# Performance work log

Measured on AMD Instinct MI355X. Metric: run time of the kernel, lower is better.

## Reference

```python
import jax, jax.numpy as jnp
import numpy as np

B, C, H, W = 32, 128, 12, 12
L = H * W
D = C + 1            # +1 coordinate channel
HID = 64

def leaky(x):
    return jax.nn.leaky_relu(x, negative_slope=0.01)

def setup_inputs() -> dict:
    key = jax.random.key(0)
    ks = jax.random.split(key, 9)
    def lin(k, fin, fout):
        bound = 1.0 / np.sqrt(fin)
        kw, kb = jax.random.split(k)
        Wt = jax.random.uniform(kw, (fin, fout), minval=-bound, maxval=bound, dtype=jnp.float32)
        bb = jax.random.uniform(kb, (fout,), minval=-bound, maxval=bound, dtype=jnp.float32)
        return Wt, bb
    x_img = jax.random.normal(ks[0], (B, C, H, W), dtype=jnp.float32)
    W1, b1 = lin(ks[1], 2 * D, HID)
    W2, b2 = lin(ks[2], HID, HID)
    Wp, bp = lin(ks[3], HID, HID)
    Wo, bo = lin(ks[4], HID, HID)
    return {"x_img": x_img, "W1": W1, "b1": b1, "W2": W2, "b2": b2,
            "Wp": Wp, "bp": bp, "Wo": Wo, "bo": bo}

def reference(x_img, W1, b1, W2, b2, Wp, bp, Wo, bo):
    b, c, h, w = x_img.shape
    length = h * w
    # [b, L, c]
    x = x_img.reshape(b, c, length).transpose(0, 2, 1)
    coords = jnp.broadcast_to(jnp.arange(length, dtype=x.dtype)[None, :, None], (b, length, 1))
    x = jnp.concatenate([x, coords], axis=2)            # [b, L, D]
    # pair feature is concat([x_i, x_j]) where x_i[b,i,j]=x[b,j], x_j[b,i,j]=x[b,i].
    # Linear on concat == split-weight sum; avoids materializing [b,L,L,2D].
    Wa, Wb = W1[:D], W1[D:]
    gi = jnp.einsum('bld,dh->blh', x, Wa)               # contribution of x_i (indexed by j)
    gj = jnp.einsum('bld,dh->blh', x, Wb)               # contribution of x_j (indexed by i)
    g = leaky(gi[:, None, :, :] + gj[:, :, None, :] + b1)   # [b, L, L, HID]
    g = leaky(jnp.einsum('bijh,hk->bijk', g, W2) + b2)       # [b, L, L, HID]
    out = g.sum(axis=(1, 2))                                 # [b, HID]
    out = leaky(out @ Wp + bp)
    out = leaky(out @ Wo + bo)
    return out
```

## Files before the change

kernel.cpp:

```cpp
#include <hip/hip_runtime.h>


#define B_   32
#define C_   128
#define L_   144
#define HID_ 64
#define D_   129
#define STR  68
#define YB_  18

typedef __bf16 bf16x8 __attribute__((ext_vector_type(8)));
typedef float  floatx4 __attribute__((ext_vector_type(4)));

__device__ __forceinline__ float leaky(float x) { return fmaxf(x, 0.01f * x); }
__device__ __forceinline__ floatx4 leaky4(floatx4 x) {
    return __builtin_elementwise_max(x, x * 0.01f);
}

__global__ __launch_bounds__(256) void k_proj(const float* __restrict__ x_img,
                                              const float* __restrict__ W1,
                                              float* __restrict__ gi,
                                              float* __restrict__ gj)
{
    int t   = threadIdx.x;
    int h   = t & 63;
    int sub = t >> 6;
    int bid = blockIdx.x;
    int b   = bid / 36;
    int l   = (bid % 36) * 4 + sub;

    const float* Wa = W1;
    const float* Wb = W1 + D_ * HID_;
    const float* xp = x_img + (size_t)(b * C_) * L_ + l;

    float ai = 0.f, aj = 0.f;
#pragma unroll 4
    for (int c = 0; c < C_; ++c) {
        float xv = xp[c * L_];
        ai = fmaf(xv, Wa[c * HID_ + h], ai);
        aj = fmaf(xv, Wb[c * HID_ + h], aj);
    }
    float fl = (float)l;
    ai = fmaf(fl, Wa[C_ * HID_ + h], ai);
    aj = fmaf(fl, Wb[C_ * HID_ + h], aj);

    int o = (b * L_ + l) * HID_ + h;
    gi[o] = ai;
    gj[o] = aj;
}

__global__ __launch_bounds__(256, 2) void k_pairs(const float* __restrict__ gi,
                                                  const float* __restrict__ gj,
                                                  const float* __restrict__ b1,
                                                  const float* __restrict__ W2,
                                                  const float* __restrict__ b2,
                                                  float* __restrict__ partial)
{
    __shared__ float smem[2 * L_ * STR];
    float* s_gi  = smem;
    float* s_gjb = smem + L_ * STR;

    const int t    = threadIdx.x;
    const int wave = t >> 6;
    const int lane = t & 63;
    const int m    = lane & 15;
    const int quad = lane >> 4;
    const int b    = blockIdx.x;

    {
        const floatx4* g4i = (const floatx4*)(gi + (size_t)b * (L_ * HID_));
        const floatx4* g4j = (const floatx4*)(gj + (size_t)b * (L_ * HID_));
        const floatx4* b14 = (const floatx4*)b1;
        for (int idx = t; idx < L_ * HID_ / 4; idx += 256) {
            int l  = idx >> 4;
            int c4 = idx & 15;
            floatx4 vi = g4i[idx];
            floatx4 vj = g4j[idx] + b14[c4];
            *(floatx4*)&s_gi [l * STR + c4 * 4] = vi;
            *(floatx4*)&s_gjb[l * STR + c4 * 4] = vj;
        }
    }

    bf16x8 Bf[2][4];
#pragma unroll
    for (int kc = 0; kc < 2; ++kc)
#pragma unroll
        for (int nt = 0; nt < 4; ++nt)
#pragma unroll
            for (int j = 0; j < 8; ++j)
                Bf[kc][nt][j] = (__bf16)W2[(kc * 32 + quad * 8 + j) * HID_ + nt * 16 + m];

    float b2v[4];
#pragma unroll
    for (int nt = 0; nt < 4; ++nt) b2v[nt] = b2[nt * 16 + m];

    floatx4 sacc[4];
#pragma unroll
    for (int nt = 0; nt < 4; ++nt) sacc[nt] = floatx4{0.f, 0.f, 0.f, 0.f};

    const int h0 = quad * 8;

    __syncthreads();

#pragma unroll
    for (int ii = 0; ii < 2; ++ii) {
        const int i = (blockIdx.y * 4 + wave) * 2 + ii;

        const float* hr = &s_gjb[i * STR];
        floatx4 gjA0 = *(const floatx4*)(hr + h0);
        floatx4 gjA1 = *(const floatx4*)(hr + h0 + 4);
        floatx4 gjB0 = *(const floatx4*)(hr + 32 + h0);
        floatx4 gjB1 = *(const floatx4*)(hr + 32 + h0 + 4);

        for (int jt = 0; jt < 9; ++jt) {
            const float* gr = &s_gi[(jt * 16 + m) * STR];

            floatx4 va0 = *(const floatx4*)(gr + h0)          + gjA0;
            floatx4 va1 = *(const floatx4*)(gr + h0 + 4)      + gjA1;
            floatx4 vb0 = *(const floatx4*)(gr + 32 + h0)     + gjB0;
            floatx4 vb1 = *(const floatx4*)(gr + 32 + h0 + 4) + gjB1;
            va0 = leaky4(va0); va1 = leaky4(va1);
            vb0 = leaky4(vb0); vb1 = leaky4(vb1);

            bf16x8 A0, A1;
#pragma unroll
            for (int j = 0; j < 4; ++j) {
                A0[j]     = (__bf16)va0[j];
                A0[4 + j] = (__bf16)va1[j];
                A1[j]     = (__bf16)vb0[j];
                A1[4 + j] = (__bf16)vb1[j];
            }

            floatx4 Cf[4];
#pragma unroll
            for (int nt = 0; nt < 4; ++nt) {
                Cf[nt] = floatx4{0.f, 0.f, 0.f, 0.f};
                Cf[nt] = __builtin_amdgcn_mfma_f32_16x16x32_bf16(A0, Bf[0][nt], Cf[nt], 0, 0, 0);
                Cf[nt] = __builtin_amdgcn_mfma_f32_16x16x32_bf16(A1, Bf[1][nt], Cf[nt], 0, 0, 0);
            }

#pragma unroll
            for (int nt = 0; nt < 4; ++nt)
                sacc[nt] += leaky4(Cf[nt] + b2v[nt]);
        }
    }

    float red[4];
#pragma unroll
    for (int nt = 0; nt < 4; ++nt) {
        float s = sacc[nt][0] + sacc[nt][1] + sacc[nt][2] + sacc[nt][3];
        s += __shfl_xor(s, 16, 64);
        s += __shfl_xor(s, 32, 64);
        red[nt] = s;
    }
    __syncthreads();
    if (quad == 0) {
#pragma unroll
        for (int nt = 0; nt < 4; ++nt)
            smem[wave * STR + nt * 16 + m] = red[nt];
    }
    __syncthreads();
    if (t < HID_) {
        float s = smem[0 * STR + t] + smem[1 * STR + t]
                + smem[2 * STR + t] + smem[3 * STR + t];
        partial[(b * YB_ + blockIdx.y) * HID_ + t] = s;
    }
}

__global__ __launch_bounds__(64) void k_mlp(const float* __restrict__ partial,
                                            const float* __restrict__ Wp,
                                            const float* __restrict__ bp,
                                            const float* __restrict__ Wo,
                                            const float* __restrict__ bo,
                                            float* __restrict__ out)
{
    __shared__ float s0[HID_], s1[HID_];
    int b = blockIdx.x, k = threadIdx.x;

    float a = 0.f;
#pragma unroll
    for (int yb = 0; yb < YB_; ++yb)
        a += partial[(b * YB_ + yb) * HID_ + k];
    s0[k] = a;
    __syncthreads();

    float v = bp[k];
#pragma unroll 8
    for (int h = 0; h < HID_; ++h) v = fmaf(s0[h], Wp[h * HID_ + k], v);
    v = leaky(v);
    s1[k] = v;
    __syncthreads();
    float w = bo[k];
#pragma unroll 8
    for (int h = 0; h < HID_; ++h) w = fmaf(s1[h], Wo[h * HID_ + k], w);
    w = leaky(w);
    out[b * HID_ + k] = w;
}

extern "C" void kernel_launch(void* const* d_in, const int* in_sizes, int n_in,
                              void* d_out, int out_size, void* d_ws, size_t ws_size,
                              hipStream_t stream)
{
    const float* x_img = (const float*)d_in[0];
    const float* W1    = (const float*)d_in[1];
    const float* b1    = (const float*)d_in[2];
    const float* W2    = (const float*)d_in[3];
    const float* b2    = (const float*)d_in[4];
    const float* Wp    = (const float*)d_in[5];
    const float* bp    = (const float*)d_in[6];
    const float* Wo    = (const float*)d_in[7];
    const float* bo    = (const float*)d_in[8];
    float* out = (float*)d_out;

    float* gi      = (float*)d_ws;
    float* gj      = gi + B_ * L_ * HID_;
    float* partial = gj + B_ * L_ * HID_;

    k_proj <<<dim3(B_ * 36), 256, 0, stream>>>(x_img, W1, gi, gj);
    k_pairs<<<dim3(B_, YB_), 256, 0, stream>>>(gi, gj, b1, W2, b2, partial);
    k_mlp  <<<dim3(B_),       64, 0, stream>>>(partial, Wp, bp, Wo, bo, out);
}
```

Before: 112.0 us.

## Stage W1 halves in LDS for projection and halve k_pairs shared memory

The projection kernel now splits the gi and gj outputs across separate blocks. Each block stages its half of W1 in shared memory and computes 12 positions, with two accumulators to expose ILP. The b1 bias is folded into gj at projection time. k_pairs no longer stages gj in LDS and instead reads its few gj rows straight from global memory. This halves its shared footprint, and launch bounds are raised to 4 blocks per CU for more occupancy. The cost is extra global reads of x_img, since each element is now read by both the gi and gj blocks, plus 33 KB of LDS per projection block.

```diff
diff --git a/kernel.cpp b/kernel.cpp
--- a/kernel.cpp
+++ b/kernel.cpp
@@ -8,6 +8,7 @@
 #define D_   129
 #define STR  68
 #define YB_  18
+#define PL_  12
 
 typedef __bf16 bf16x8 __attribute__((ext_vector_type(8)));
 typedef float  floatx4 __attribute__((ext_vector_type(4)));
@@ -19,46 +20,52 @@
 
 __global__ __launch_bounds__(256) void k_proj(const float* __restrict__ x_img,
                                               const float* __restrict__ W1,
+                                              const float* __restrict__ b1,
                                               float* __restrict__ gi,
-                                              float* __restrict__ gj)
-{
-    int t   = threadIdx.x;
-    int h   = t & 63;
-    int sub = t >> 6;
-    int bid = blockIdx.x;
-    int b   = bid / 36;
-    int l   = (bid % 36) * 4 + sub;
-
-    const float* Wa = W1;
-    const float* Wb = W1 + D_ * HID_;
-    const float* xp = x_img + (size_t)(b * C_) * L_ + l;
-
-    float ai = 0.f, aj = 0.f;
+                                              float* __restrict__ gjb)
+{
+    __shared__ float sW[D_ * HID_];
+    const int t     = threadIdx.x;
+    const int b     = blockIdx.x >> 1;
+    const int which = blockIdx.x & 1;
+    const int l0    = blockIdx.y * PL_;
+
+    {
+        const floatx4* w4 = (const floatx4*)(W1 + which * (D_ * HID_));
+        floatx4* s4 = (floatx4*)sW;
+        for (int idx = t; idx < D_ * HID_ / 4; idx += 256)
+            s4[idx] = w4[idx];
+    }
+    __syncthreads();
+
+    const int h    = t & 63;
+    const int wave = t >> 6;
+    float* outp  = which ? gjb : gi;
+    const float bias = which ? b1[h] : 0.f;
+
+#pragma unroll
+    for (int il = 0; il < PL_ / 4; ++il) {
+        const int l = l0 + wave * (PL_ / 4) + il;
+        const float* xp = x_img + (size_t)(b * C_) * L_ + l;
+
+        float a0 = fmaf((float)l, sW[C_ * HID_ + h], bias);
+        float a1 = 0.f;
 #pragma unroll 4
-    for (int c = 0; c < C_; ++c) {
-        float xv = xp[c * L_];
-        ai = fmaf(xv, Wa[c * HID_ + h], ai);
-        aj = fmaf(xv, Wb[c * HID_ + h], aj);
-    }
-    float fl = (float)l;
-    ai = fmaf(fl, Wa[C_ * HID_ + h], ai);
-    aj = fmaf(fl, Wb[C_ * HID_ + h], aj);
-
-    int o = (b * L_ + l) * HID_ + h;
-    gi[o] = ai;
-    gj[o] = aj;
-}
-
-__global__ __launch_bounds__(256, 2) void k_pairs(const float* __restrict__ gi,
-                                                  const float* __restrict__ gj,
-                                                  const float* __restrict__ b1,
+        for (int c = 0; c < C_; c += 2) {
+            a0 = fmaf(xp[c * L_],       sW[c * HID_ + h],       a0);
+            a1 = fmaf(xp[(c + 1) * L_], sW[(c + 1) * HID_ + h], a1);
+        }
+        outp[(b * L_ + l) * HID_ + h] = a0 + a1;
+    }
+}
+
+__global__ __launch_bounds__(256, 4) void k_pairs(const float* __restrict__ gi,
+                                                  const float* __restrict__ gjb,
                                                   const float* __restrict__ W2,
                                                   const float* __restrict__ b2,
                                                   float* __restrict__ partial)
 {
-    __shared__ float smem[2 * L_ * STR];
-    float* s_gi  = smem;
-    float* s_gjb = smem + L_ * STR;
+    __shared__ float s_gi[L_ * STR];
 
     const int t    = threadIdx.x;
     const int wave = t >> 6;
@@ -69,15 +76,10 @@
 
     {
         const floatx4* g4i = (const floatx4*)(gi + (size_t)b * (L_ * HID_));
-        const floatx4* g4j = (const floatx4*)(gj + (size_t)b * (L_ * HID_));
-        const floatx4* b14 = (const floatx4*)b1;
         for (int idx = t; idx < L_ * HID_ / 4; idx += 256) {
             int l  = idx >> 4;
             int c4 = idx & 15;
-            floatx4 vi = g4i[idx];
-            floatx4 vj = g4j[idx] + b14[c4];
-            *(floatx4*)&s_gi [l * STR + c4 * 4] = vi;
-            *(floatx4*)&s_gjb[l * STR + c4 * 4] = vj;
+            *(floatx4*)&s_gi[l * STR + c4 * 4] = g4i[idx];
         }
     }
 
@@ -106,11 +108,11 @@
     for (int ii = 0; ii < 2; ++ii) {
         const int i = (blockIdx.y * 4 + wave) * 2 + ii;
 
-        const float* hr = &s_gjb[i * STR];
-        floatx4 gjA0 = *(const floatx4*)(hr + h0);
-        floatx4 gjA1 = *(const floatx4*)(hr + h0 + 4);
-        floatx4 gjB0 = *(const floatx4*)(hr + 32 + h0);
-        floatx4 gjB1 = *(const floatx4*)(hr + 32 + h0 + 4);
+        const float* gjr = gjb + ((size_t)b * L_ + i) * HID_;
+        floatx4 gjA0 = *(const floatx4*)(gjr + h0);
+        floatx4 gjA1 = *(const floatx4*)(gjr + h0 + 4);
+        floatx4 gjB0 = *(const floatx4*)(gjr + 32 + h0);
+        floatx4 gjB1 = *(const floatx4*)(gjr + 32 + h0 + 4);
 
         for (int jt = 0; jt < 9; ++jt) {
             const float* gr = &s_gi[(jt * 16 + m) * STR];
@@ -157,12 +159,12 @@
     if (quad == 0) {
 #pragma unroll
         for (int nt = 0; nt < 4; ++nt)
-            smem[wave * STR + nt * 16 + m] = red[nt];
+            s_gi[wave * STR + nt * 16 + m] = red[nt];
     }
     __syncthreads();
     if (t < HID_) {
-        float s = smem[0 * STR + t] + smem[1 * STR + t]
-                + smem[2 * STR + t] + smem[3 * STR + t];
+        float s = s_gi[0 * STR + t] + s_gi[1 * STR + t]
+                + s_gi[2 * STR + t] + s_gi[3 * STR + t];
         partial[(b * YB_ + blockIdx.y) * HID_ + t] = s;
     }
 }
@@ -213,10 +215,10 @@
     float* out = (float*)d_out;
 
     float* gi      = (float*)d_ws;
-    float* gj      = gi + B_ * L_ * HID_;
-    float* partial = gj + B_ * L_ * HID_;
-
-    k_proj <<<dim3(B_ * 36), 256, 0, stream>>>(x_img, W1, gi, gj);
-    k_pairs<<<dim3(B_, YB_), 256, 0, stream>>>(gi, gj, b1, W2, b2, partial);
-    k_mlp  <<<dim3(B_),       64, 0, stream>>>(partial, Wp, bp, Wo, bo, out);
-}
+    float* gjb     = gi + B_ * L_ * HID_;
+    float* partial = gjb + B_ * L_ * HID_;
+
+    k_proj <<<dim3(B_ * 2, L_ / PL_), 256, 0, stream>>>(x_img, W1, b1, gi, gjb);
+    k_pairs<<<dim3(B_, YB_),          256, 0, stream>>>(gi, gjb, W2, b2, partial);
+    k_mlp  <<<dim3(B_),                64, 0, stream>>>(partial, Wp, bp, Wo, bo, out);
+}
```

Result: faster. 106.3 us (median of 2 runs) (-5.1%).
